# Optimization experiments

Measured on AMD Instinct MI355X. Metric: run time of the kernel, lower is better.

Reference implementation:

```python
import jax, jax.numpy as jnp
import numpy as np

ALPHA = 0.2          # leaky relu negative slope
SCALE_ATT = 1.0
NEG_MASK = -9e15


def setup_inputs() -> dict:
    key = jax.random.key(0)
    k1, k2, k3, k4 = jax.random.split(key, 4)
    B, N, Din, Dout = 32, 1024, 256, 256
    h = jax.random.normal(k1, (B, N, Din), dtype=jnp.float32)
    adj = jax.random.randint(k2, (B, N, N), 0, 2, dtype=jnp.int32)
    W = jax.random.normal(k3, (Dout, Din), dtype=jnp.float32) * (1.0 / np.sqrt(Din))
    b = jnp.zeros((Dout,), dtype=jnp.float32)
    a = jax.random.normal(k4, (2 * Dout,), dtype=jnp.float32) * 0.1
    return {"h": h, "adj": adj, "W": W, "b": b, "a": a}


def reference(h, adj, W, b, a):
    # z: [B, N, Dout]
    z = jnp.einsum('bnd,od->bno', h, W) + b
    Dout = z.shape[-1]
    a1, a2 = a[:Dout], a[Dout:]
    # a^T [z_i || z_j] = a1.z_i + a2.z_j  (same math as the N^2 concat)
    s1 = jnp.einsum('bnd,d->bn', z, a1)  # source score per node
    s2 = jnp.einsum('bnd,d->bn', z, a2)  # target score per node
    e = jax.nn.leaky_relu(s1[:, :, None] + s2[:, None, :], negative_slope=ALPHA)
    e = jnp.where(adj > 0, e, NEG_MASK) * SCALE_ATT
    attention = jax.nn.softmax(e, axis=-1)   # [B, N, N]
    # dropout p=0 / eval mode: no-op
    h_prime = jnp.einsum('bij,bjd->bid', attention, z)
    return jax.nn.elu(h_prime)
```

## Files before the change

kernel.cpp:

```cpp
#include <hip/hip_runtime.h>
#include <math.h>

#define LRELU_ALPHA 0.2f
#define NEG_MASK_V -9000000000000000.0f

typedef __attribute__((ext_vector_type(8))) short short8;
typedef __attribute__((ext_vector_type(4))) float floatx4;
typedef __attribute__((ext_vector_type(8))) unsigned short u16x8;
typedef __attribute__((ext_vector_type(4))) unsigned short u16x4;

__device__ __forceinline__ unsigned short f2bf(float x) {
  union { float f; unsigned u; } v; v.f = x;
  unsigned r = v.u + 0x7fff + ((v.u >> 16) & 1);
  return (unsigned short)(r >> 16);
}

__global__ __launch_bounds__(256) void prep_kernel(
    const float* __restrict__ W, const float* __restrict__ b,
    const float* __restrict__ a, unsigned short* __restrict__ Wb,
    float* __restrict__ u1, float* __restrict__ u2, float* __restrict__ cst)
{
  const int t = threadIdx.x;
  if (blockIdx.x == 0) {
    float a1s = 0.f, a2s = 0.f;
    for (int o = 0; o < 256; ++o) {
      const float w = W[o * 256 + t];
      a1s = fmaf(w, a[o], a1s);
      a2s = fmaf(w, a[256 + o], a2s);
    }
    u1[t] = a1s; u2[t] = a2s;
    if (t < 64) {
      float p1 = 0.f, p2 = 0.f;
      #pragma unroll
      for (int q = 0; q < 4; ++q) {
        const float bv = b[t + q * 64];
        p1 = fmaf(bv, a[t + q * 64], p1);
        p2 = fmaf(bv, a[256 + t + q * 64], p2);
      }
      #pragma unroll
      for (int off = 32; off > 0; off >>= 1) {
        p1 += __shfl_xor(p1, off); p2 += __shfl_xor(p2, off);
      }
      if (t == 0) { cst[0] = p1; cst[1] = p2; }
    }
  } else {
    const int base = (blockIdx.x - 1) * 2048 + t * 8;
    const float4 v0 = *(const float4*)&W[base];
    const float4 v1 = *(const float4*)&W[base + 4];
    u16x8 o;
    o[0] = f2bf(v0.x); o[1] = f2bf(v0.y); o[2] = f2bf(v0.z); o[3] = f2bf(v0.w);
    o[4] = f2bf(v1.x); o[5] = f2bf(v1.y); o[6] = f2bf(v1.z); o[7] = f2bf(v1.w);
    *(u16x8*)&Wb[base] = o;
  }
}

__global__ __launch_bounds__(256) void sdot_kernel(
    const float* __restrict__ h, const float* __restrict__ u1,
    const float* __restrict__ u2, const float* __restrict__ cst,
    float* __restrict__ s1, float* __restrict__ s2)
{
  const int t = threadIdx.x, l = t & 63, w = t >> 6;
  const long row0 = (long)blockIdx.x * 64 + w * 16;
  const float4 u1v = *(const float4*)&u1[l * 4];
  const float4 u2v = *(const float4*)&u2[l * 4];
  const float c1 = cst[0], c2 = cst[1];
  #pragma unroll
  for (int r = 0; r < 16; ++r) {
    const float4 hv = *(const float4*)&h[(row0 + r) * 256 + l * 4];
    float d1 = hv.x * u1v.x + hv.y * u1v.y + hv.z * u1v.z + hv.w * u1v.w;
    float d2 = hv.x * u2v.x + hv.y * u2v.y + hv.z * u2v.z + hv.w * u2v.w;
    #pragma unroll
    for (int off = 32; off > 0; off >>= 1) {
      d1 += __shfl_xor(d1, off); d2 += __shfl_xor(d2, off);
    }
    if (l == 0) { s1[row0 + r] = d1 + c1; s2[row0 + r] = d2 + c2; }
  }
}

__global__ __launch_bounds__(256) void zmfma_kernel(
    const float* __restrict__ h, const unsigned short* __restrict__ Wb,
    const float* __restrict__ bias, unsigned short* __restrict__ zf)
{
  __shared__ __align__(16) unsigned char smem[46080];
  unsigned short (*h_tile)[72] = (unsigned short(*)[72])smem;
  unsigned short (*w_tile)[72] = (unsigned short(*)[72])(smem + 9216);
  unsigned short (*ztile)[68]  = (unsigned short(*)[68])smem;

  const int t = threadIdx.x, l = t & 63, w = t >> 6;
  const int bi = blockIdx.x;
  const long row0 = (long)bi * 64;

  floatx4 acc[4][4];
  #pragma unroll
  for (int mf = 0; mf < 4; ++mf)
    #pragma unroll
    for (int nf = 0; nf < 4; ++nf) acc[mf][nf] = (floatx4)0.f;

  for (int k0 = 0; k0 < 256; k0 += 64) {
    __syncthreads();
    #pragma unroll
    for (int p = 0; p < 4; ++p) {
      const int row = p * 16 + (t >> 4);
      const float4 hv = *(const float4*)&h[(row0 + row) * 256 + k0 + (t & 15) * 4];
      u16x4 hb;
      hb[0] = f2bf(hv.x); hb[1] = f2bf(hv.y); hb[2] = f2bf(hv.z); hb[3] = f2bf(hv.w);
      *(u16x4*)&h_tile[row][(t & 15) * 4] = hb;
    }
    #pragma unroll
    for (int p = 0; p < 8; ++p) {
      const int o = p * 32 + (t >> 3);
      const u16x8 wv = *(const u16x8*)&Wb[o * 256 + k0 + (t & 7) * 8];
      *(u16x8*)&w_tile[o][(t & 7) * 8] = wv;
    }
    __syncthreads();

    #pragma unroll
    for (int kk = 0; kk < 2; ++kk) {
      short8 af[4];
      #pragma unroll
      for (int mf = 0; mf < 4; ++mf)
        af[mf] = *(const short8*)&h_tile[mf * 16 + (l & 15)][kk * 32 + (l >> 4) * 8];
      #pragma unroll
      for (int nf = 0; nf < 4; ++nf) {
        const short8 bf = *(const short8*)&w_tile[w * 64 + nf * 16 + (l & 15)][kk * 32 + (l >> 4) * 8];
        #pragma unroll
        for (int mf = 0; mf < 4; ++mf)
          acc[mf][nf] = __builtin_amdgcn_mfma_f32_16x16x32_bf16(af[mf], bf, acc[mf][nf], 0, 0, 0);
      }
    }
  }

  __syncthreads();
  #pragma unroll
  for (int nf = 0; nf < 4; ++nf) {
    const int o = w * 64 + nf * 16 + (l & 15);
    const float bv = bias[o];
    #pragma unroll
    for (int mf = 0; mf < 4; ++mf) {
      u16x4 zv;
      #pragma unroll
      for (int rg = 0; rg < 4; ++rg) zv[rg] = f2bf(acc[mf][nf][rg] + bv);
      *(u16x4*)&ztile[o][mf * 16 + (l >> 4) * 4] = zv;
    }
  }
  __syncthreads();
  #pragma unroll
  for (int seg = 0; seg < 8; ++seg)
    *(u16x8*)&zf[((size_t)bi * 8 + seg) * 2048 + t * 8] =
        *(const u16x8*)&ztile[t][seg * 8];
}

__global__ __launch_bounds__(512, 4) void attn_kernel(
    const unsigned short* __restrict__ zf, const float* __restrict__ s1g,
    const float* __restrict__ s2g, const int* __restrict__ adj,
    float* __restrict__ out)
{
  __shared__ unsigned short p_lds[64][72];
  __shared__ float s2s[1024];
  __shared__ float s1s[64];
  __shared__ float sum_lds[64];

  const int t = threadIdx.x;
  const int l = t & 63;
  const int w = t >> 6;

  const int wg = blockIdx.x;
  const int sw = (wg & 7) * 64 + (wg >> 3);
  const int b = sw >> 4;
  const int i0 = (sw & 15) * 64;

  const int i_loc = t >> 3;
  const int jb = (t & 7) * 8;

  const size_t adj_base = (size_t)b * 1024 * 1024 + (size_t)(i0 + i_loc) * 1024 + jb;
  const size_t zf_batch = (size_t)b * 16 * 16384;
  const size_t zf_lane  = (size_t)(l >> 4) * 2048 + (size_t)(w * 32 + (l & 15)) * 8;

  if (t < 64) s1s[t] = s1g[b * 1024 + i0 + t];
  s2s[t] = s2g[b * 1024 + t];
  s2s[512 + t] = s2g[b * 1024 + 512 + t];

  floatx4 acc[4][2];
  #pragma unroll
  for (int mf = 0; mf < 4; ++mf) {
    acc[mf][0] = (floatx4)0.f;
    acc[mf][1] = (floatx4)0.f;
  }
  float sm = 0.f;

  int4 ac0 = *(const int4*)&adj[adj_base];
  int4 ac1 = *(const int4*)&adj[adj_base + 4];

  short8 vz[2][4];
  {
    const unsigned short* zp = zf + zf_batch + zf_lane;
    vz[0][0] = *(const short8*)(zp);
    vz[0][1] = *(const short8*)(zp + 128);
    vz[0][2] = *(const short8*)(zp + 8192);
    vz[0][3] = *(const short8*)(zp + 8320);
  }
  __syncthreads();

  for (int jt2 = 0; jt2 < 1024; jt2 += 128) {
    #pragma unroll
    for (int ph = 0; ph < 2; ++ph) {
      const int jt = jt2 + ph * 64;

      const float s1v = s1s[i_loc];
      const float4 s2a = *(const float4*)&s2s[jt + jb];
      const float4 s2b = *(const float4*)&s2s[jt + jb + 4];
      float e[8] = {s2a.x, s2a.y, s2a.z, s2a.w, s2b.x, s2b.y, s2b.z, s2b.w};
      const int am[8] = {ac0.x, ac0.y, ac0.z, ac0.w, ac1.x, ac1.y, ac1.z, ac1.w};
      #pragma unroll
      for (int q = 0; q < 8; ++q) {
        float x = s1v + e[q];
        x = fmaxf(x, LRELU_ALPHA * x);
        e[q] = am[q] > 0 ? x : NEG_MASK_V;
      }

      if (jt + 64 < 1024) {
        ac0 = *(const int4*)&adj[adj_base + jt + 64];
        ac1 = *(const int4*)&adj[adj_base + jt + 68];
        const unsigned short* zp =
            zf + zf_batch + (size_t)((jt >> 6) + 1) * 16384 + zf_lane;
        vz[ph ^ 1][0] = *(const short8*)(zp);
        vz[ph ^ 1][1] = *(const short8*)(zp + 128);
        vz[ph ^ 1][2] = *(const short8*)(zp + 8192);
        vz[ph ^ 1][3] = *(const short8*)(zp + 8320);
      }

      u16x8 pk;
      #pragma unroll
      for (int q = 0; q < 8; ++q) {
        const float p = __expf(e[q]);
        sm += p;
        pk[q] = f2bf(p);
      }

      __syncthreads();
      *(u16x8*)&p_lds[i_loc][jb] = pk;
      __syncthreads();

      #pragma unroll
      for (int kk = 0; kk < 2; ++kk) {
        #pragma unroll
        for (int mf = 0; mf < 4; ++mf) {
          const short8 af =
              *(const short8*)&p_lds[mf * 16 + (l & 15)][kk * 32 + (l >> 4) * 8];
          acc[mf][0] = __builtin_amdgcn_mfma_f32_16x16x32_bf16(
              af, vz[ph][kk * 2 + 0], acc[mf][0], 0, 0, 0);
          acc[mf][1] = __builtin_amdgcn_mfma_f32_16x16x32_bf16(
              af, vz[ph][kk * 2 + 1], acc[mf][1], 0, 0, 0);
        }
      }
    }
  }

  sm += __shfl_xor(sm, 1);
  sm += __shfl_xor(sm, 2);
  sm += __shfl_xor(sm, 4);
  if ((t & 7) == 0) sum_lds[i_loc] = sm;
  __syncthreads();

  const size_t obase = ((size_t)b * 1024 + i0) * 256 + w * 32;
  #pragma unroll
  for (int mf = 0; mf < 4; ++mf) {
    const int rbase = mf * 16 + ((l >> 4) << 2);
    #pragma unroll
    for (int rg = 0; rg < 4; ++rg) {
      const float inv = 1.0f / sum_lds[rbase + rg];
      #pragma unroll
      for (int nf = 0; nf < 2; ++nf) {
        float v = acc[mf][nf][rg] * inv;
        v = v > 0.f ? v : expm1f(v);
        out[obase + (size_t)(rbase + rg) * 256 + nf * 16 + (l & 15)] = v;
      }
    }
  }
}

extern "C" void kernel_launch(void* const* d_in, const int* in_sizes, int n_in,
                              void* d_out, int out_size, void* d_ws, size_t ws_size,
                              hipStream_t stream) {
  const float* h    = (const float*)d_in[0];
  const int*   adj  = (const int*)d_in[1];
  const float* W    = (const float*)d_in[2];
  const float* bias = (const float*)d_in[3];
  const float* a    = (const float*)d_in[4];
  float* out = (float*)d_out;

  unsigned short* zf = (unsigned short*)d_ws;
  float* s1  = (float*)((char*)d_ws + 16777216);
  float* s2  = (float*)((char*)d_ws + 16908288);
  float* u1  = (float*)((char*)d_ws + 17039360);
  float* u2  = (float*)((char*)d_ws + 17040384);
  float* cst = (float*)((char*)d_ws + 17041408);
  unsigned short* Wb = (unsigned short*)((char*)d_ws + 17825792);

  prep_kernel<<<dim3(33), dim3(256), 0, stream>>>(W, bias, a, Wb, u1, u2, cst);
  sdot_kernel<<<dim3(512), dim3(256), 0, stream>>>(h, u1, u2, cst, s1, s2);
  zmfma_kernel<<<dim3(512), dim3(256), 0, stream>>>(h, Wb, bias, zf);
  attn_kernel<<<dim3(512), dim3(512), 0, stream>>>(zf, s1, s2, adj, out);
}
```

Before: 71.30 us.

## Fuse score dot products into projection GEMM and double-buffer attention LDS

The separate sdot kernel is removed. The per-node attention scores s1/s2 are now computed inside the z projection kernel from the same h loads used for the bf16 tile, which saves one launch and a second full read of h. The attention kernel double-buffers the probability tile in LDS so each step needs one barrier instead of two. Scalar bf16 rounding is replaced by the packed v_cvt_pk_bf16_f32 instruction, and the s1 load is hoisted out of the loop. This adds register pressure in the GEMM kernel and relies on hand-placed waitcnt/barrier asm being correct.

Measured after the change: 75.85 us. 6.4% more time.

```diff
diff --git a/kernel.cpp b/kernel.cpp
--- a/kernel.cpp
+++ b/kernel.cpp
@@ -13,6 +13,12 @@
   union { float f; unsigned u; } v; v.f = x;
   unsigned r = v.u + 0x7fff + ((v.u >> 16) & 1);
   return (unsigned short)(r >> 16);
+}
+
+__device__ __forceinline__ unsigned cvt_pk_bf16(float lo, float hi) {
+  unsigned r;
+  asm("v_cvt_pk_bf16_f32 %0, %1, %2" : "=v"(r) : "v"(lo), "v"(hi));
+  return r;
 }
 
 __global__ __launch_bounds__(256) void prep_kernel(
@@ -23,6 +29,7 @@
   const int t = threadIdx.x;
   if (blockIdx.x == 0) {
     float a1s = 0.f, a2s = 0.f;
+    #pragma unroll 4
     for (int o = 0; o < 256; ++o) {
       const float w = W[o * 256 + t];
       a1s = fmaf(w, a[o], a1s);
@@ -54,32 +61,12 @@
   }
 }
 
-__global__ __launch_bounds__(256) void sdot_kernel(
-    const float* __restrict__ h, const float* __restrict__ u1,
-    const float* __restrict__ u2, const float* __restrict__ cst,
-    float* __restrict__ s1, float* __restrict__ s2)
-{
-  const int t = threadIdx.x, l = t & 63, w = t >> 6;
-  const long row0 = (long)blockIdx.x * 64 + w * 16;
-  const float4 u1v = *(const float4*)&u1[l * 4];
-  const float4 u2v = *(const float4*)&u2[l * 4];
-  const float c1 = cst[0], c2 = cst[1];
-  #pragma unroll
-  for (int r = 0; r < 16; ++r) {
-    const float4 hv = *(const float4*)&h[(row0 + r) * 256 + l * 4];
-    float d1 = hv.x * u1v.x + hv.y * u1v.y + hv.z * u1v.z + hv.w * u1v.w;
-    float d2 = hv.x * u2v.x + hv.y * u2v.y + hv.z * u2v.z + hv.w * u2v.w;
-    #pragma unroll
-    for (int off = 32; off > 0; off >>= 1) {
-      d1 += __shfl_xor(d1, off); d2 += __shfl_xor(d2, off);
-    }
-    if (l == 0) { s1[row0 + r] = d1 + c1; s2[row0 + r] = d2 + c2; }
-  }
-}
-
 __global__ __launch_bounds__(256) void zmfma_kernel(
     const float* __restrict__ h, const unsigned short* __restrict__ Wb,
-    const float* __restrict__ bias, unsigned short* __restrict__ zf)
+    const float* __restrict__ bias, const float* __restrict__ u1,
+    const float* __restrict__ u2, const float* __restrict__ cst,
+    unsigned short* __restrict__ zf, float* __restrict__ s1,
+    float* __restrict__ s2)
 {
   __shared__ __align__(16) unsigned char smem[46080];
   unsigned short (*h_tile)[72] = (unsigned short(*)[72])smem;
@@ -96,15 +83,23 @@
     #pragma unroll
     for (int nf = 0; nf < 4; ++nf) acc[mf][nf] = (floatx4)0.f;
 
+  float d1a[4] = {0.f, 0.f, 0.f, 0.f};
+  float d2a[4] = {0.f, 0.f, 0.f, 0.f};
+
   for (int k0 = 0; k0 < 256; k0 += 64) {
     __syncthreads();
+    const float4 u1v = *(const float4*)&u1[k0 + (t & 15) * 4];
+    const float4 u2v = *(const float4*)&u2[k0 + (t & 15) * 4];
     #pragma unroll
     for (int p = 0; p < 4; ++p) {
       const int row = p * 16 + (t >> 4);
       const float4 hv = *(const float4*)&h[(row0 + row) * 256 + k0 + (t & 15) * 4];
-      u16x4 hb;
-      hb[0] = f2bf(hv.x); hb[1] = f2bf(hv.y); hb[2] = f2bf(hv.z); hb[3] = f2bf(hv.w);
-      *(u16x4*)&h_tile[row][(t & 15) * 4] = hb;
+      d1a[p] = fmaf(hv.x, u1v.x, fmaf(hv.y, u1v.y, fmaf(hv.z, u1v.z, fmaf(hv.w, u1v.w, d1a[p]))));
+      d2a[p] = fmaf(hv.x, u2v.x, fmaf(hv.y, u2v.y, fmaf(hv.z, u2v.z, fmaf(hv.w, u2v.w, d2a[p]))));
+      uint2 hb;
+      hb.x = cvt_pk_bf16(hv.x, hv.y);
+      hb.y = cvt_pk_bf16(hv.z, hv.w);
+      *(uint2*)&h_tile[row][(t & 15) * 4] = hb;
     }
     #pragma unroll
     for (int p = 0; p < 8; ++p) {
@@ -130,6 +125,22 @@
     }
   }
 
+  {
+    const float c1 = cst[0], c2 = cst[1];
+    #pragma unroll
+    for (int p = 0; p < 4; ++p) {
+      float d1 = d1a[p], d2 = d2a[p];
+      #pragma unroll
+      for (int off = 8; off > 0; off >>= 1) {
+        d1 += __shfl_xor(d1, off); d2 += __shfl_xor(d2, off);
+      }
+      if ((t & 15) == 0) {
+        const long row = row0 + p * 16 + (t >> 4);
+        s1[row] = d1 + c1; s2[row] = d2 + c2;
+      }
+    }
+  }
+
   __syncthreads();
   #pragma unroll
   for (int nf = 0; nf < 4; ++nf) {
@@ -137,10 +148,10 @@
     const float bv = bias[o];
     #pragma unroll
     for (int mf = 0; mf < 4; ++mf) {
-      u16x4 zv;
-      #pragma unroll
-      for (int rg = 0; rg < 4; ++rg) zv[rg] = f2bf(acc[mf][nf][rg] + bv);
-      *(u16x4*)&ztile[o][mf * 16 + (l >> 4) * 4] = zv;
+      uint2 zv;
+      zv.x = cvt_pk_bf16(acc[mf][nf][0] + bv, acc[mf][nf][1] + bv);
+      zv.y = cvt_pk_bf16(acc[mf][nf][2] + bv, acc[mf][nf][3] + bv);
+      *(uint2*)&ztile[o][mf * 16 + (l >> 4) * 4] = zv;
     }
   }
   __syncthreads();
@@ -155,7 +166,7 @@
     const float* __restrict__ s2g, const int* __restrict__ adj,
     float* __restrict__ out)
 {
-  __shared__ unsigned short p_lds[64][72];
+  __shared__ unsigned short p_lds[2][64][72];
   __shared__ float s2s[1024];
   __shared__ float s1s[64];
   __shared__ float sum_lds[64];
@@ -200,13 +211,13 @@
     vz[0][3] = *(const short8*)(zp + 8320);
   }
   __syncthreads();
+  const float s1v = s1s[i_loc];
 
   for (int jt2 = 0; jt2 < 1024; jt2 += 128) {
     #pragma unroll
     for (int ph = 0; ph < 2; ++ph) {
       const int jt = jt2 + ph * 64;
 
-      const float s1v = s1s[i_loc];
       const float4 s2a = *(const float4*)&s2s[jt + jb];
       const float4 s2b = *(const float4*)&s2s[jt + jb + 4];
       float e[8] = {s2a.x, s2a.y, s2a.z, s2a.w, s2b.x, s2b.y, s2b.z, s2b.w};
@@ -229,24 +240,26 @@
         vz[ph ^ 1][3] = *(const short8*)(zp + 8320);
       }
 
-      u16x8 pk;
-      #pragma unroll
-      for (int q = 0; q < 8; ++q) {
-        const float p = __expf(e[q]);
-        sm += p;
-        pk[q] = f2bf(p);
-      }
-
-      __syncthreads();
-      *(u16x8*)&p_lds[i_loc][jb] = pk;
-      __syncthreads();
+      float p[8];
+      #pragma unroll
+      for (int q = 0; q < 8; ++q) { p[q] = __expf(e[q]); sm += p[q]; }
+      uint4 pk;
+      pk.x = cvt_pk_bf16(p[0], p[1]);
+      pk.y = cvt_pk_bf16(p[2], p[3]);
+      pk.z = cvt_pk_bf16(p[4], p[5]);
+      pk.w = cvt_pk_bf16(p[6], p[7]);
+      *(uint4*)&p_lds[ph][i_loc][jb] = pk;
+
+      asm volatile("s_waitcnt lgkmcnt(0)" ::: "memory");
+      __builtin_amdgcn_s_barrier();
+      asm volatile("" ::: "memory");
 
       #pragma unroll
       for (int kk = 0; kk < 2; ++kk) {
         #pragma unroll
         for (int mf = 0; mf < 4; ++mf) {
           const short8 af =
-              *(const short8*)&p_lds[mf * 16 + (l & 15)][kk * 32 + (l >> 4) * 8];
+              *(const short8*)&p_lds[ph][mf * 16 + (l & 15)][kk * 32 + (l >> 4) * 8];
           acc[mf][0] = __builtin_amdgcn_mfma_f32_16x16x32_bf16(
               af, vz[ph][kk * 2 + 0], acc[mf][0], 0, 0, 0);
           acc[mf][1] = __builtin_amdgcn_mfma_f32_16x16x32_bf16(
@@ -298,7 +311,6 @@
   unsigned short* Wb = (unsigned short*)((char*)d_ws + 17825792);
 
   prep_kernel<<<dim3(33), dim3(256), 0, stream>>>(W, bias, a, Wb, u1, u2, cst);
-  sdot_kernel<<<dim3(512), dim3(256), 0, stream>>>(h, u1, u2, cst, s1, s2);
-  zmfma_kernel<<<dim3(512), dim3(256), 0, stream>>>(h, Wb, bias, zf);
+  zmfma_kernel<<<dim3(512), dim3(256), 0, stream>>>(h, Wb, bias, u1, u2, cst, zf, s1, s2);
   attn_kernel<<<dim3(512), dim3(512), 0, stream>>>(zf, s1, s2, adj, out);
 }
```

## Double-buffer attention P tile in LDS, prefetch adjacency two tiles ahead

Applied to the files above, without the earlier changes.

The attention loop now double-buffers the P tile in LDS, indexed by phase, so each iteration needs one barrier instead of two. The adjacency mask is prefetched two 64-column tiles ahead rather than one, and the s1 load is hoisted out of the loop. The manual bf16 rounding is replaced by the hardware v_cvt_pk_bf16_f32 instruction, and setprio is raised around the MFMA block. The aim is to cut barrier stalls and load latency, at the cost of more LDS and registers, which may reduce occupancy.

Measured after the change: 76.31 us. 7.0% more time.

```diff
diff --git a/kernel.cpp b/kernel.cpp
--- a/kernel.cpp
+++ b/kernel.cpp
@@ -13,6 +13,12 @@
   union { float f; unsigned u; } v; v.f = x;
   unsigned r = v.u + 0x7fff + ((v.u >> 16) & 1);
   return (unsigned short)(r >> 16);
+}
+
+__device__ __forceinline__ unsigned cvt_pk_bf16(float lo, float hi) {
+  unsigned r;
+  asm("v_cvt_pk_bf16_f32 %0, %1, %2" : "=v"(r) : "v"(lo), "v"(hi));
+  return r;
 }
 
 __global__ __launch_bounds__(256) void prep_kernel(
@@ -23,6 +29,7 @@
   const int t = threadIdx.x;
   if (blockIdx.x == 0) {
     float a1s = 0.f, a2s = 0.f;
+    #pragma unroll 4
     for (int o = 0; o < 256; ++o) {
       const float w = W[o * 256 + t];
       a1s = fmaf(w, a[o], a1s);
@@ -137,10 +144,10 @@
     const float bv = bias[o];
     #pragma unroll
     for (int mf = 0; mf < 4; ++mf) {
-      u16x4 zv;
-      #pragma unroll
-      for (int rg = 0; rg < 4; ++rg) zv[rg] = f2bf(acc[mf][nf][rg] + bv);
-      *(u16x4*)&ztile[o][mf * 16 + (l >> 4) * 4] = zv;
+      uint2 zv;
+      zv.x = cvt_pk_bf16(acc[mf][nf][0] + bv, acc[mf][nf][1] + bv);
+      zv.y = cvt_pk_bf16(acc[mf][nf][2] + bv, acc[mf][nf][3] + bv);
+      *(uint2*)&ztile[o][mf * 16 + (l >> 4) * 4] = zv;
     }
   }
   __syncthreads();
@@ -155,7 +162,7 @@
     const float* __restrict__ s2g, const int* __restrict__ adj,
     float* __restrict__ out)
 {
-  __shared__ unsigned short p_lds[64][72];
+  __shared__ unsigned short p_lds[2][64][72];
   __shared__ float s2s[1024];
   __shared__ float s1s[64];
   __shared__ float sum_lds[64];
@@ -188,8 +195,11 @@
   }
   float sm = 0.f;
 
-  int4 ac0 = *(const int4*)&adj[adj_base];
-  int4 ac1 = *(const int4*)&adj[adj_base + 4];
+  int4 ac[2][2];
+  ac[0][0] = *(const int4*)&adj[adj_base];
+  ac[0][1] = *(const int4*)&adj[adj_base + 4];
+  ac[1][0] = *(const int4*)&adj[adj_base + 64];
+  ac[1][1] = *(const int4*)&adj[adj_base + 68];
 
   short8 vz[2][4];
   {
@@ -200,17 +210,18 @@
     vz[0][3] = *(const short8*)(zp + 8320);
   }
   __syncthreads();
+  const float s1v = s1s[i_loc];
 
   for (int jt2 = 0; jt2 < 1024; jt2 += 128) {
     #pragma unroll
     for (int ph = 0; ph < 2; ++ph) {
       const int jt = jt2 + ph * 64;
 
-      const float s1v = s1s[i_loc];
       const float4 s2a = *(const float4*)&s2s[jt + jb];
       const float4 s2b = *(const float4*)&s2s[jt + jb + 4];
+      const int4 a0 = ac[ph][0], a1 = ac[ph][1];
       float e[8] = {s2a.x, s2a.y, s2a.z, s2a.w, s2b.x, s2b.y, s2b.z, s2b.w};
-      const int am[8] = {ac0.x, ac0.y, ac0.z, ac0.w, ac1.x, ac1.y, ac1.z, ac1.w};
+      const int am[8] = {a0.x, a0.y, a0.z, a0.w, a1.x, a1.y, a1.z, a1.w};
       #pragma unroll
       for (int q = 0; q < 8; ++q) {
         float x = s1v + e[q];
@@ -218,9 +229,11 @@
         e[q] = am[q] > 0 ? x : NEG_MASK_V;
       }
 
+      if (jt + 128 < 1024) {
+        ac[ph][0] = *(const int4*)&adj[adj_base + jt + 128];
+        ac[ph][1] = *(const int4*)&adj[adj_base + jt + 132];
+      }
       if (jt + 64 < 1024) {
-        ac0 = *(const int4*)&adj[adj_base + jt + 64];
-        ac1 = *(const int4*)&adj[adj_base + jt + 68];
         const unsigned short* zp =
             zf + zf_batch + (size_t)((jt >> 6) + 1) * 16384 + zf_lane;
         vz[ph ^ 1][0] = *(const short8*)(zp);
@@ -229,30 +242,34 @@
         vz[ph ^ 1][3] = *(const short8*)(zp + 8320);
       }
 
-      u16x8 pk;
-      #pragma unroll
-      for (int q = 0; q < 8; ++q) {
-        const float p = __expf(e[q]);
-        sm += p;
-        pk[q] = f2bf(p);
-      }
-
-      __syncthreads();
-      *(u16x8*)&p_lds[i_loc][jb] = pk;
-      __syncthreads();
-
+      float p[8];
+      #pragma unroll
+      for (int q = 0; q < 8; ++q) { p[q] = __expf(e[q]); sm += p[q]; }
+      uint4 pk;
+      pk.x = cvt_pk_bf16(p[0], p[1]);
+      pk.y = cvt_pk_bf16(p[2], p[3]);
+      pk.z = cvt_pk_bf16(p[4], p[5]);
+      pk.w = cvt_pk_bf16(p[6], p[7]);
+      *(uint4*)&p_lds[ph][i_loc][jb] = pk;
+
+      asm volatile("s_waitcnt lgkmcnt(0)" ::: "memory");
+      __builtin_amdgcn_s_barrier();
+      __builtin_amdgcn_sched_barrier(0);
+
+      __builtin_amdgcn_s_setprio(1);
       #pragma unroll
       for (int kk = 0; kk < 2; ++kk) {
         #pragma unroll
         for (int mf = 0; mf < 4; ++mf) {
           const short8 af =
-              *(const short8*)&p_lds[mf * 16 + (l & 15)][kk * 32 + (l >> 4) * 8];
+              *(const short8*)&p_lds[ph][mf * 16 + (l & 15)][kk * 32 + (l >> 4) * 8];
           acc[mf][0] = __builtin_amdgcn_mfma_f32_16x16x32_bf16(
               af, vz[ph][kk * 2 + 0], acc[mf][0], 0, 0, 0);
           acc[mf][1] = __builtin_amdgcn_mfma_f32_16x16x32_bf16(
               af, vz[ph][kk * 2 + 1], acc[mf][1], 0, 0, 0);
         }
       }
+      __builtin_amdgcn_s_setprio(0);
     }
   }
 
```
